# Kernel optimization log

Measured on AMD Instinct MI355X. Metric: run time of the kernel, lower is better.

Reference implementation:

```python
import jax, jax.numpy as jnp
import numpy as np

B, S, E, NH = 2, 1024, 2048, 16
DH = E // NH
EPS = 1e-6

def setup_inputs() -> dict:
    key = jax.random.key(0)
    ks = jax.random.split(key, 6)
    q = jax.random.normal(ks[0], (B, S, E), dtype=jnp.float32)
    k = jax.random.normal(ks[1], (B, S, E), dtype=jnp.float32)
    v = jax.random.normal(ks[2], (B, S, E), dtype=jnp.float32)
    Wi = jax.random.normal(ks[3], (3 * E, NH), dtype=jnp.float32) * 0.02
    bi = jax.random.normal(ks[4], (NH,), dtype=jnp.float32) * 0.1
    Wf = jax.random.normal(ks[5], (3 * E, NH), dtype=jnp.float32) * 0.02
    bf = jnp.linspace(3.0, 6.0, NH, dtype=jnp.float32)  # bias_linspace_initializer(3,6)
    ln_scale = jnp.ones((E,), dtype=jnp.float32)
    return {"q": q, "k": k, "v": v, "Wi": Wi, "bi": bi, "Wf": Wf, "bf": bf, "ln_scale": ln_scale}

def _mlstm_forward(q, k, v, Wi, bi, Wf, bf, ln_scale):
    b, s, e = q.shape
    nh = Wi.shape[1]
    dh = e // nh
    x = jnp.concatenate([q, k, v], axis=-1)                     # (B,S,3E)
    ig = (x @ Wi + bi).transpose(0, 2, 1)[..., None]            # (B,NH,S,1)
    fg = (x @ Wf + bf).transpose(0, 2, 1)[..., None]            # (B,NH,S,1)
    split = lambda t: t.reshape(b, s, nh, dh).transpose(0, 2, 1, 3)
    qh, kh, vh = split(q), split(k), split(v)                   # (B,NH,S,DH)
    # parallel_stabilized_simple backend
    log_f = jax.nn.log_sigmoid(fg)                              # (B,NH,S,1)
    log_f_cum = jnp.concatenate(
        [jnp.zeros((b, nh, 1, 1), q.dtype), jnp.cumsum(log_f, axis=2)], axis=2
    )                                                           # (B,NH,S+1,1)
    # D[i,j] = cumsum[i] - cumsum[j] on causal part
    fg_mat = log_f_cum - jnp.transpose(log_f_cum, (0, 1, 3, 2)) # (B,NH,S+1,S+1)
    ltr = jnp.tril(jnp.ones((s, s), dtype=bool))
    log_fg = jnp.where(ltr, fg_mat[:, :, 1:, 1:], -jnp.inf)     # (B,NH,S,S)
    log_D = log_fg + jnp.transpose(ig, (0, 1, 3, 2))            # + i_j per column
    max_log_D = jnp.max(log_D, axis=-1, keepdims=True)          # (B,NH,S,1)
    D = jnp.exp(log_D - max_log_D)
    qk = jnp.einsum('bhsd,bhtd->bhst', qh, kh) / jnp.sqrt(jnp.asarray(dh, q.dtype))
    C = qk * D                                                  # (B,NH,S,S)
    normalizer = jnp.maximum(jnp.abs(C.sum(-1, keepdims=True)), jnp.exp(-max_log_D))
    Cn = C / (normalizer + EPS)
    h = jnp.einsum('bhst,bhtd->bhsd', Cn, vh)                   # (B,NH,S,DH)
    # MultiHeadLayerNorm: normalize over DH per head, scale (no bias)
    mu = h.mean(-1, keepdims=True)
    var = ((h - mu) ** 2).mean(-1, keepdims=True)
    hn = (h - mu) * jax.lax.rsqrt(var + EPS)
    hn = hn * ln_scale.reshape(1, nh, 1, dh)
    return hn.transpose(0, 2, 1, 3).reshape(b, s, e)            # (B,S,E)

def reference(q, k, v, Wi, bi, Wf, bf, ln_scale):
    return _mlstm_forward(q, k, v, Wi, bi, Wf, bf, ln_scale)
```

## Files before the change

### kernel.cpp

```cpp
#include <hip/hip_runtime.h>
#include <hip/hip_bf16.h>

#define B_   2
#define S_   1024
#define E_   2048
#define NH_  16
#define DH_  128
#define EPS_ 1e-6f

using half8   = __attribute__((ext_vector_type(8))) _Float16;
using floatx4 = __attribute__((ext_vector_type(4))) float;

__device__ __forceinline__ half8 cvt8h(const float* __restrict__ p) {
    float4 a = *(const float4*)p;
    float4 b = *(const float4*)(p + 4);
    half8 r;
    r[0] = (_Float16)a.x; r[1] = (_Float16)a.y;
    r[2] = (_Float16)a.z; r[3] = (_Float16)a.w;
    r[4] = (_Float16)b.x; r[5] = (_Float16)b.y;
    r[6] = (_Float16)b.z; r[7] = (_Float16)b.w;
    return r;
}

__global__ __launch_bounds__(256, 4) void gates_kernel(
    const float* __restrict__ q, const float* __restrict__ k,
    const float* __restrict__ v, const float* __restrict__ Wi,
    const float* __restrict__ Wf, float* __restrict__ pre_i,
    float* __restrict__ pre_f, _Float16* __restrict__ qhg,
    _Float16* __restrict__ khg, _Float16* __restrict__ vtg)
{
    __shared__ __attribute__((aligned(16))) _Float16 xs[32 * 264];
    __shared__ __attribute__((aligned(16))) _Float16 wt[32 * 264];

    const int t    = threadIdx.x;
    const int w    = t >> 6, lane = t & 63, quad = lane >> 4, l15 = lane & 15;
    const int mw   = w & 1, nw = w >> 1;
    const int m0   = blockIdx.x * 32;
    const int by   = blockIdx.y;
    const int kbase = by * 768;
    const int bblk = m0 >> 10;
    const int s0   = m0 & 1023;

    floatx4 acc = {0.f, 0.f, 0.f, 0.f};

    for (int c = 0; c < 3; ++c) {
        __syncthreads();
        const int e0   = kbase + c * 256;
        const int tsel = e0 >> 11;
        const int el0  = e0 & 2047;
        const float* xb = (tsel == 0) ? q : (tsel == 1) ? k : v;
        _Float16* fout = (tsel == 0) ? qhg : khg;
        #pragma unroll
        for (int i = 0; i < 4; ++i) {
            int g = t + i * 256;
            int row = g >> 5, grp = g & 31;
            half8 s8 = cvt8h(xb + (size_t)(m0 + row) * E_ + el0 + grp * 8);
            *(half8*)(&xs[row * 264 + grp * 8]) = s8;
            if (tsel < 2) {
                int el = el0 + grp * 8;
                int h  = el >> 7, d = el & 127;
                *(half8*)(fout + ((size_t)(bblk * NH_ + h) * S_ + s0 + row) * DH_ + d) = s8;
            }
        }
        {
            const int kk = t;
            const float* wiRow = Wi + (size_t)(e0 + kk) * NH_;
            const float* wfRow = Wf + (size_t)(e0 + kk) * NH_;
            float wif[16], wff[16];
            #pragma unroll
            for (int i4 = 0; i4 < 4; ++i4) {
                float4 a = *(const float4*)(wiRow + i4 * 4);
                wif[i4*4+0]=a.x; wif[i4*4+1]=a.y; wif[i4*4+2]=a.z; wif[i4*4+3]=a.w;
                float4 b = *(const float4*)(wfRow + i4 * 4);
                wff[i4*4+0]=b.x; wff[i4*4+1]=b.y; wff[i4*4+2]=b.z; wff[i4*4+3]=b.w;
            }
            #pragma unroll
            for (int hh = 0; hh < 16; ++hh) wt[hh * 264 + kk]        = (_Float16)wif[hh];
            #pragma unroll
            for (int hh = 0; hh < 16; ++hh) wt[(16 + hh) * 264 + kk] = (_Float16)wff[hh];
        }
        __syncthreads();
        if (tsel == 2) {
            const int col = t;
            const int el  = el0 + col;
            const int h   = el >> 7, d = el & 127;
            _Float16 tmp[32];
            #pragma unroll
            for (int r = 0; r < 32; ++r) tmp[r] = xs[r * 264 + col];
            const size_t vo = ((size_t)(bblk * NH_ + h) * DH_ + d) * S_ + s0;
            #pragma unroll
            for (int i = 0; i < 4; ++i)
                *(half8*)(vtg + vo + i * 8) = *(half8*)(&tmp[i * 8]);
        }
        #pragma unroll
        for (int ks = 0; ks < 8; ++ks) {
            half8 af = *(const half8*)(&xs[(mw * 16 + l15) * 264 + ks * 32 + quad * 8]);
            half8 bw = *(const half8*)(&wt[(nw * 16 + l15) * 264 + ks * 32 + quad * 8]);
            acc = __builtin_amdgcn_mfma_f32_16x16x32_f16(af, bw, acc, 0, 0, 0);
        }
    }
    #pragma unroll
    for (int reg = 0; reg < 4; ++reg) {
        int m   = m0 + mw * 16 + quad * 4 + reg;
        int b   = m >> 10, s = m & 1023;
        int col = nw * 16 + l15;
        float vacc = acc[reg];
        if (col < 16)
            pre_i[((size_t)(by * 32 + b * NH_ + col)) * S_ + s] = vacc;
        else
            pre_f[((size_t)(by * 32 + b * NH_ + col - 16)) * S_ + s] = vacc;
    }
}

__global__ __launch_bounds__(256, 2) void attn_kernel(
    const _Float16* __restrict__ qh, const _Float16* __restrict__ kh,
    const _Float16* __restrict__ vtg, const float* __restrict__ pre_i,
    const float* __restrict__ pre_f, const float* __restrict__ bi,
    const float* __restrict__ bfb, const float* __restrict__ lnsc,
    float* __restrict__ out)
{
    __shared__ __attribute__((aligned(16))) _Float16 Pb[2][64 * 72];
    __shared__ __attribute__((aligned(16))) float ajAll[1024];
    __shared__ float cq64[64], nf64[64];
    __shared__ float wsum[4], wmax[4];
    __shared__ float lpart[2][2][32];
    __shared__ float spart[2][2][32];
    __shared__ float qpart[2][2][32];

    const int t    = threadIdx.x;
    const int w    = t >> 6, lane = t & 63, quad = lane >> 4, l15 = lane & 15;
    const int mw   = w & 1, nw = w >> 1;
    const int L    = blockIdx.x;
    int qi, bh;
    if (L < 256) { qi = L >> 5;                bh = L & 31; }
    else         { qi = 15 - ((L - 256) >> 5); bh = (L - 256) & 31; }
    const int b    = bh >> 4, h = bh & 15;
    const int q0   = qi * 64;

    const _Float16* kfb = kh  + ((size_t)bh * S_  + nw * 32 + l15) * DH_ + quad * 8;
    const _Float16* vfb = vtg + ((size_t)bh * DH_ + nw * 64 + l15) * S_ + quad * 8;

    half8 kcur[4][2], vcur[2][4];
    #pragma unroll
    for (int n = 0; n < 2; ++n)
        #pragma unroll
        for (int ks = 0; ks < 4; ++ks)
            kcur[ks][n] = *(const half8*)(kfb + n * 16 * DH_ + ks * 32);
    #pragma unroll
    for (int n = 0; n < 4; ++n)
        #pragma unroll
        for (int ks2 = 0; ks2 < 2; ++ks2)
            vcur[ks2][n] = *(const half8*)(vfb + n * 16 * S_ + ks2 * 32);
    half8 aq[2][4];
    #pragma unroll
    for (int s = 0; s < 2; ++s) {
        const _Float16* qrow = qh + ((size_t)bh * S_ + q0 + mw * 32 + s * 16 + l15) * DH_;
        #pragma unroll
        for (int ks = 0; ks < 4; ++ks)
            aq[s][ks] = *(const half8*)(qrow + ks * 32 + quad * 8);
    }

    {
        const int e4 = t * 4;
        const float bih = bi[h], bfh = bfb[h];
        float ig4[4] = {bih, bih, bih, bih};
        float x4[4]  = {bfh, bfh, bfh, bfh};
        #pragma unroll
        for (int y = 0; y < 8; ++y) {
            float4 pi = *(const float4*)(pre_i + ((size_t)(y * 32 + bh)) * S_ + e4);
            float4 pf = *(const float4*)(pre_f + ((size_t)(y * 32 + bh)) * S_ + e4);
            ig4[0] += pi.x; ig4[1] += pi.y; ig4[2] += pi.z; ig4[3] += pi.w;
            x4[0]  += pf.x; x4[1]  += pf.y; x4[2]  += pf.z; x4[3]  += pf.w;
        }
        float lf[4], ls = 0.f;
        #pragma unroll
        for (int e = 0; e < 4; ++e) {
            float x = x4[e];
            float l = (x >= 0.f) ? -log1pf(__expf(-x)) : (x - log1pf(__expf(x)));
            ls += l; lf[e] = ls;
        }
        float sc = ls;
        #pragma unroll
        for (int off = 1; off < 64; off <<= 1) {
            float o = __shfl_up(sc, off);
            if (lane >= off) sc += o;
        }
        float sexcl = sc - ls;
        if (lane == 63) wsum[w] = sc;
        __syncthreads();
        float Foff = 0.f;
        for (int i = 0; i < w; ++i) Foff += wsum[i];
        float Fbase = Foff + sexcl;
        float av[4], lm[4], am = -3.0e38f;
        #pragma unroll
        for (int e = 0; e < 4; ++e) {
            float F = Fbase + lf[e];
            float a = ig4[e] - F;
            av[e] = a; am = fmaxf(am, a); lm[e] = am;
        }
        *(float4*)(&ajAll[e4]) = *(float4*)av;
        float msc = am;
        #pragma unroll
        for (int off = 1; off < 64; off <<= 1) {
            float o = __shfl_up(msc, off);
            if (lane >= off) msc = fmaxf(msc, o);
        }
        float mprev = __shfl_up(msc, 1);
        float mexcl = (lane == 0) ? -3.0e38f : mprev;
        if (lane == 63) wmax[w] = msc;
        __syncthreads();
        float Moff = -3.0e38f;
        for (int i = 0; i < w; ++i) Moff = fmaxf(Moff, wmax[i]);
        float Mbase = fmaxf(Moff, mexcl);
        #pragma unroll
        for (int e = 0; e < 4; ++e) {
            int s = e4 + e;
            if (s >= q0 && s < q0 + 64) {
                float M = fmaxf(Mbase, lm[e]);
                float F = Fbase + lf[e];
                cq64[s - q0] = -M;
                nf64[s - q0] = expf(fminf(-(F + M), 80.f));
            }
        }
    }
    __syncthreads();

    float ci_r[2][4], nfv_r[2][4];
    #pragma unroll
    for (int s = 0; s < 2; ++s)
        #pragma unroll
        for (int reg = 0; reg < 4; ++reg) {
            int rr = mw * 32 + s * 16 + quad * 4 + reg;
            ci_r[s][reg]  = cq64[rr];
            nfv_r[s][reg] = nf64[rr];
        }

    floatx4 acc_h[2][4];
    #pragma unroll
    for (int s = 0; s < 2; ++s)
        #pragma unroll
        for (int i = 0; i < 4; ++i) acc_h[s][i] = (floatx4){0.f, 0.f, 0.f, 0.f};
    float lrun[2][4] = {{0.f, 0.f, 0.f, 0.f}, {0.f, 0.f, 0.f, 0.f}};
    const float rscale = 0.08838834764831845f;

    for (int kt = 0; kt <= qi; ++kt) {
        const bool diag = (kt == qi);
        floatx4 sacc[2][2];
        #pragma unroll
        for (int s = 0; s < 2; ++s)
            #pragma unroll
            for (int n = 0; n < 2; ++n) sacc[s][n] = (floatx4){0.f, 0.f, 0.f, 0.f};
        if (!(diag && mw == 0 && nw == 1)) {
            __builtin_amdgcn_s_setprio(1);
            #pragma unroll
            for (int ks = 0; ks < 4; ++ks) {
                #pragma unroll
                for (int n = 0; n < 2; ++n) {
                    sacc[0][n] = __builtin_amdgcn_mfma_f32_16x16x32_f16(aq[0][ks], kcur[ks][n], sacc[0][n], 0, 0, 0);
                    sacc[1][n] = __builtin_amdgcn_mfma_f32_16x16x32_f16(aq[1][ks], kcur[ks][n], sacc[1][n], 0, 0, 0);
                }
            }
            __builtin_amdgcn_s_setprio(0);
        }
        if (kt < qi) {
            const _Float16* kp = kfb + (size_t)(kt + 1) * 64 * DH_;
            #pragma unroll
            for (int n = 0; n < 2; ++n)
                #pragma unroll
                for (int ks = 0; ks < 4; ++ks)
                    kcur[ks][n] = *(const half8*)(kp + n * 16 * DH_ + ks * 32);
        }
        _Float16* pb = &Pb[kt & 1][0];
        #pragma unroll
        for (int n = 0; n < 2; ++n) {
            int jl = nw * 32 + n * 16 + l15;
            float a_j = ajAll[kt * 64 + jl];
            #pragma unroll
            for (int s = 0; s < 2; ++s) {
                #pragma unroll
                for (int reg = 0; reg < 4; ++reg) {
                    int rloc = mw * 32 + s * 16 + quad * 4 + reg;
                    float p = 0.f;
                    if (!diag || (jl <= rloc))
                        p = sacc[s][n][reg] * rscale * __expf(fminf(ci_r[s][reg] + a_j, 0.f));
                    lrun[s][reg] += p;
                    pb[rloc * 72 + jl] = (_Float16)p;
                }
            }
        }
        __syncthreads();

        __builtin_amdgcn_s_setprio(1);
        #pragma unroll
        for (int ks2 = 0; ks2 < 2; ++ks2) {
            half8 ap0 = *(const half8*)(&pb[(mw * 32 + l15) * 72 + ks2 * 32 + quad * 8]);
            half8 ap1 = *(const half8*)(&pb[(mw * 32 + 16 + l15) * 72 + ks2 * 32 + quad * 8]);
            #pragma unroll
            for (int n = 0; n < 4; ++n) {
                acc_h[0][n] = __builtin_amdgcn_mfma_f32_16x16x32_f16(ap0, vcur[ks2][n], acc_h[0][n], 0, 0, 0);
                acc_h[1][n] = __builtin_amdgcn_mfma_f32_16x16x32_f16(ap1, vcur[ks2][n], acc_h[1][n], 0, 0, 0);
            }
        }
        __builtin_amdgcn_s_setprio(0);
        if (kt < qi) {
            const _Float16* vp = vfb + (size_t)(kt + 1) * 64;
            #pragma unroll
            for (int n = 0; n < 4; ++n)
                #pragma unroll
                for (int ks2 = 0; ks2 < 2; ++ks2)
                    vcur[ks2][n] = *(const half8*)(vp + n * 16 * S_ + ks2 * 32);
        }
    }

    #pragma unroll
    for (int s = 0; s < 2; ++s)
        #pragma unroll
        for (int reg = 0; reg < 4; ++reg) {
            float l = lrun[s][reg];
            l += __shfl_xor(l, 1); l += __shfl_xor(l, 2);
            l += __shfl_xor(l, 4); l += __shfl_xor(l, 8);
            if (l15 == 0) lpart[nw][mw][s * 16 + quad * 4 + reg] = l;
        }
    __syncthreads();
    float inv_r[2][4];
    #pragma unroll
    for (int s = 0; s < 2; ++s)
        #pragma unroll
        for (int reg = 0; reg < 4; ++reg) {
            int rr = s * 16 + quad * 4 + reg;
            float ltot = lpart[0][mw][rr] + lpart[1][mw][rr];
            inv_r[s][reg] = 1.f / (fmaxf(fabsf(ltot), nfv_r[s][reg]) + EPS_);
        }
    #pragma unroll
    for (int s = 0; s < 2; ++s)
        #pragma unroll
        for (int reg = 0; reg < 4; ++reg) {
            float sum = 0.f, sq = 0.f;
            #pragma unroll
            for (int n = 0; n < 4; ++n) {
                float x = acc_h[s][n][reg] * inv_r[s][reg];
                sum += x; sq += x * x;
            }
            sum += __shfl_xor(sum, 1); sq += __shfl_xor(sq, 1);
            sum += __shfl_xor(sum, 2); sq += __shfl_xor(sq, 2);
            sum += __shfl_xor(sum, 4); sq += __shfl_xor(sq, 4);
            sum += __shfl_xor(sum, 8); sq += __shfl_xor(sq, 8);
            if (l15 == 0) {
                spart[nw][mw][s * 16 + quad * 4 + reg] = sum;
                qpart[nw][mw][s * 16 + quad * 4 + reg] = sq;
            }
        }
    __syncthreads();
    #pragma unroll
    for (int s = 0; s < 2; ++s)
        #pragma unroll
        for (int reg = 0; reg < 4; ++reg) {
            int rr   = s * 16 + quad * 4 + reg;
            float sum = spart[0][mw][rr] + spart[1][mw][rr];
            float sq  = qpart[0][mw][rr] + qpart[1][mw][rr];
            float mean = sum * (1.f / 128.f);
            float var  = fmaxf(sq * (1.f / 128.f) - mean * mean, 0.f);
            float rstd = rsqrtf(var + EPS_);
            int rl = q0 + mw * 32 + rr;
            size_t orow = ((size_t)b * S_ + rl) * E_ + h * DH_;
            #pragma unroll
            for (int n = 0; n < 4; ++n) {
                int d = nw * 64 + n * 16 + l15;
                out[orow + d] = (acc_h[s][n][reg] * inv_r[s][reg] - mean) * rstd * lnsc[h * DH_ + d];
            }
        }
}

extern "C" void kernel_launch(void* const* d_in, const int* in_sizes, int n_in,
                              void* d_out, int out_size, void* d_ws, size_t ws_size,
                              hipStream_t stream)
{
    const float* q    = (const float*)d_in[0];
    const float* k    = (const float*)d_in[1];
    const float* v    = (const float*)d_in[2];
    const float* Wi   = (const float*)d_in[3];
    const float* bi   = (const float*)d_in[4];
    const float* Wf   = (const float*)d_in[5];
    const float* bfb  = (const float*)d_in[6];
    const float* lnsc = (const float*)d_in[7];
    float* out        = (float*)d_out;

    const int NS  = B_ * NH_ * S_;
    float* pre_i = (float*)d_ws;
    float* pre_f = pre_i + 8 * NS;
    _Float16* qh  = (_Float16*)(pre_f + 8 * NS);
    _Float16* kh  = qh + (size_t)32 * S_ * DH_;
    _Float16* vtg = kh + (size_t)32 * S_ * DH_;

    gates_kernel<<<dim3(64, 8), 256, 0, stream>>>(q, k, v, Wi, Wf, pre_i, pre_f,
                                                  qh, kh, vtg);
    attn_kernel<<<dim3(512), 256, 0, stream>>>(qh, kh, vtg, pre_i, pre_f,
                                               bi, bfb, lnsc, out);
}
```

Before: 152.8 us.

## Split attention key range across two blocks with atomic-flag partial merge

```diff
diff --git a/kernel.cpp b/kernel.cpp
--- a/kernel.cpp
+++ b/kernel.cpp
@@ -27,12 +27,17 @@
     const float* __restrict__ v, const float* __restrict__ Wi,
     const float* __restrict__ Wf, float* __restrict__ pre_i,
     float* __restrict__ pre_f, _Float16* __restrict__ qhg,
-    _Float16* __restrict__ khg, _Float16* __restrict__ vtg)
+    _Float16* __restrict__ khg, _Float16* __restrict__ vtg,
+    unsigned int* __restrict__ pflags)
 {
     __shared__ __attribute__((aligned(16))) _Float16 xs[32 * 264];
     __shared__ __attribute__((aligned(16))) _Float16 wt[32 * 264];
 
     const int t    = threadIdx.x;
+    if (blockIdx.x == 0 && blockIdx.y == 0) {
+        pflags[t]       = 0u;
+        pflags[t + 256] = 0u;
+    }
     const int w    = t >> 6, lane = t & 63, quad = lane >> 4, l15 = lane & 15;
     const int mw   = w & 1, nw = w >> 1;
     const int m0   = blockIdx.x * 32;
@@ -112,12 +117,13 @@
     }
 }
 
-__global__ __launch_bounds__(256, 2) void attn_kernel(
+__global__ __launch_bounds__(256, 4) void attn_kernel(
     const _Float16* __restrict__ qh, const _Float16* __restrict__ kh,
     const _Float16* __restrict__ vtg, const float* __restrict__ pre_i,
     const float* __restrict__ pre_f, const float* __restrict__ bi,
     const float* __restrict__ bfb, const float* __restrict__ lnsc,
-    float* __restrict__ out)
+    float* __restrict__ out, float* __restrict__ pws,
+    unsigned int* __restrict__ pflags)
 {
     __shared__ __attribute__((aligned(16))) _Float16 Pb[2][64 * 72];
     __shared__ __attribute__((aligned(16))) float ajAll[1024];
@@ -126,31 +132,40 @@
     __shared__ float lpart[2][2][32];
     __shared__ float spart[2][2][32];
     __shared__ float qpart[2][2][32];
+    __shared__ int oldf_sh;
 
     const int t    = threadIdx.x;
     const int w    = t >> 6, lane = t & 63, quad = lane >> 4, l15 = lane & 15;
     const int mw   = w & 1, nw = w >> 1;
     const int L    = blockIdx.x;
-    int qi, bh;
-    if (L < 256) { qi = L >> 5;                bh = L & 31; }
-    else         { qi = 15 - ((L - 256) >> 5); bh = (L - 256) & 31; }
+    const int u    = L & 255, sel = L >> 8;
+    const int bh   = u & 31, qp = u >> 5;
+    const int qt   = (sel < 2) ? qp : (15 - qp);
+    const int half = sel & 1;
+    const int ntiles = qt + 1, hA = (ntiles + 1) >> 1;
+    const int k0   = half ? hA : 0, k1 = half ? ntiles : hA;
+    const int pid  = bh * 16 + qt;
     const int b    = bh >> 4, h = bh & 15;
-    const int q0   = qi * 64;
+    const int q0   = qt * 64;
 
     const _Float16* kfb = kh  + ((size_t)bh * S_  + nw * 32 + l15) * DH_ + quad * 8;
     const _Float16* vfb = vtg + ((size_t)bh * DH_ + nw * 64 + l15) * S_ + quad * 8;
 
     half8 kcur[4][2], vcur[2][4];
-    #pragma unroll
-    for (int n = 0; n < 2; ++n)
-        #pragma unroll
-        for (int ks = 0; ks < 4; ++ks)
-            kcur[ks][n] = *(const half8*)(kfb + n * 16 * DH_ + ks * 32);
-    #pragma unroll
-    for (int n = 0; n < 4; ++n)
-        #pragma unroll
-        for (int ks2 = 0; ks2 < 2; ++ks2)
-            vcur[ks2][n] = *(const half8*)(vfb + n * 16 * S_ + ks2 * 32);
+    {
+        const _Float16* kp = kfb + (size_t)k0 * 64 * DH_;
+        const _Float16* vp = vfb + (size_t)k0 * 64;
+        #pragma unroll
+        for (int n = 0; n < 2; ++n)
+            #pragma unroll
+            for (int ks = 0; ks < 4; ++ks)
+                kcur[ks][n] = *(const half8*)(kp + n * 16 * DH_ + ks * 32);
+        #pragma unroll
+        for (int n = 0; n < 4; ++n)
+            #pragma unroll
+            for (int ks2 = 0; ks2 < 2; ++ks2)
+                vcur[ks2][n] = *(const half8*)(vp + n * 16 * S_ + ks2 * 32);
+    }
     half8 aq[2][4];
     #pragma unroll
     for (int s = 0; s < 2; ++s) {
@@ -243,8 +258,8 @@
     float lrun[2][4] = {{0.f, 0.f, 0.f, 0.f}, {0.f, 0.f, 0.f, 0.f}};
     const float rscale = 0.08838834764831845f;
 
-    for (int kt = 0; kt <= qi; ++kt) {
-        const bool diag = (kt == qi);
+    for (int kt = k0; kt < k1; ++kt) {
+        const bool diag = (kt == qt);
         floatx4 sacc[2][2];
         #pragma unroll
         for (int s = 0; s < 2; ++s)
@@ -262,7 +277,7 @@
             }
             __builtin_amdgcn_s_setprio(0);
         }
-        if (kt < qi) {
+        if (kt + 1 < k1) {
             const _Float16* kp = kfb + (size_t)(kt + 1) * 64 * DH_;
             #pragma unroll
             for (int n = 0; n < 2; ++n)
@@ -302,13 +317,47 @@
             }
         }
         __builtin_amdgcn_s_setprio(0);
-        if (kt < qi) {
+        if (kt + 1 < k1) {
             const _Float16* vp = vfb + (size_t)(kt + 1) * 64;
             #pragma unroll
             for (int n = 0; n < 4; ++n)
                 #pragma unroll
                 for (int ks2 = 0; ks2 < 2; ++ks2)
                     vcur[ks2][n] = *(const half8*)(vp + n * 16 * S_ + ks2 * 32);
+        }
+    }
+
+    {
+        float* base = pws + ((size_t)((pid << 1) | half) * 256 + t) * 40;
+        #pragma unroll
+        for (int s = 0; s < 2; ++s)
+            #pragma unroll
+            for (int n = 0; n < 4; ++n)
+                *(floatx4*)(base + (s * 4 + n) * 4) = acc_h[s][n];
+        #pragma unroll
+        for (int s = 0; s < 2; ++s) {
+            floatx4 lv = {lrun[s][0], lrun[s][1], lrun[s][2], lrun[s][3]};
+            *(floatx4*)(base + 32 + s * 4) = lv;
+        }
+    }
+    __threadfence();
+    __syncthreads();
+    if (t == 0) oldf_sh = (int)atomicAdd(&pflags[pid], 1u);
+    __syncthreads();
+    if (oldf_sh == 0) return;
+    __threadfence();
+    {
+        const float* pbase = pws + ((size_t)((pid << 1) | (half ^ 1)) * 256 + t) * 40;
+        #pragma unroll
+        for (int s = 0; s < 2; ++s)
+            #pragma unroll
+            for (int n = 0; n < 4; ++n)
+                acc_h[s][n] += *(const floatx4*)(pbase + (s * 4 + n) * 4);
+        #pragma unroll
+        for (int s = 0; s < 2; ++s) {
+            floatx4 lv = *(const floatx4*)(pbase + 32 + s * 4);
+            lrun[s][0] += lv[0]; lrun[s][1] += lv[1];
+            lrun[s][2] += lv[2]; lrun[s][3] += lv[3];
         }
     }
 
@@ -391,9 +440,11 @@
     _Float16* qh  = (_Float16*)(pre_f + 8 * NS);
     _Float16* kh  = qh + (size_t)32 * S_ * DH_;
     _Float16* vtg = kh + (size_t)32 * S_ * DH_;
+    float* pws    = (float*)(vtg + (size_t)32 * DH_ * S_);
+    unsigned int* pflags = (unsigned int*)(pws + (size_t)1024 * 256 * 40);
 
     gates_kernel<<<dim3(64, 8), 256, 0, stream>>>(q, k, v, Wi, Wf, pre_i, pre_f,
-                                                  qh, kh, vtg);
-    attn_kernel<<<dim3(512), 256, 0, stream>>>(qh, kh, vtg, pre_i, pre_f,
-                                               bi, bfb, lnsc, out);
+                                                  qh, kh, vtg, pflags);
+    attn_kernel<<<dim3(1024), 256, 0, stream>>>(qh, kh, vtg, pre_i, pre_f,
+                                                bi, bfb, lnsc, out, pws, pflags);
 }
```

Measured after the change: 535.2 us. 3.5x slower.
